# Optimization experiments

Hardware: AMD Instinct MI355X
Metric: run time of the kernel (lower is better)

Reference implementation:

```python
import jax, jax.numpy as jnp
import numpy as np

N = 10000        # nodes
E = 160000       # edges (before self loops)
F_IN = 4         # n_features
D = 128          # d_model (per-head out channels for GAT, GCN width)
H = 8            # n_heads
NEG_SLOPE = 0.2  # PyG GATConv default leaky relu slope


def setup_inputs() -> dict:
    key = jax.random.key(0)
    ks = jax.random.split(key, 10)
    x = jax.random.normal(ks[0], (N, F_IN), dtype=jnp.float32)
    edge_index = jax.random.randint(ks[1], (2, E), 0, N, dtype=jnp.int64)
    s = 0.05
    gat_w = jax.random.normal(ks[2], (F_IN, H * D), dtype=jnp.float32) * s
    att_src = jax.random.normal(ks[3], (H, D), dtype=jnp.float32) * s
    att_dst = jax.random.normal(ks[4], (H, D), dtype=jnp.float32) * s
    gat_b = jnp.zeros((H * D,), dtype=jnp.float32)
    gcn1_w = jax.random.normal(ks[5], (H * D, D), dtype=jnp.float32) * s
    gcn1_b = jnp.zeros((D,), dtype=jnp.float32)
    gcn2_w = jax.random.normal(ks[6], (D, D), dtype=jnp.float32) * s
    gcn2_b = jnp.zeros((D,), dtype=jnp.float32)
    return {"x": x, "edge_index": edge_index, "gat_w": gat_w,
            "att_src": att_src, "att_dst": att_dst, "gat_b": gat_b,
            "gcn1_w": gcn1_w, "gcn1_b": gcn1_b,
            "gcn2_w": gcn2_w, "gcn2_b": gcn2_b}


def _add_self_loops(edge_index, n):
    loops = jnp.arange(n, dtype=edge_index.dtype)
    src = jnp.concatenate([edge_index[0], loops])
    dst = jnp.concatenate([edge_index[1], loops])
    return src, dst


def _gat_conv(x, src, dst, w, att_src, att_dst, b):
    # PyG GATConv, concat=True: h [N,H,D]
    h = (x @ w).reshape(-1, H, D)
    a_s = jnp.einsum('nhd,hd->nh', h, att_src)   # per-node src score
    a_d = jnp.einsum('nhd,hd->nh', h, att_dst)   # per-node dst score
    e = jax.nn.leaky_relu(a_s[src] + a_d[dst], NEG_SLOPE)  # [Etot,H]
    # segment softmax over destination node, per head
    m = jax.ops.segment_max(e, dst, num_segments=N)
    ex = jnp.exp(e - m[dst])
    denom = jax.ops.segment_sum(ex, dst, num_segments=N)
    alpha = ex / denom[dst]                       # [Etot,H]
    msg = h[src] * alpha[:, :, None]              # [Etot,H,D]
    out = jax.ops.segment_sum(msg, dst, num_segments=N)  # [N,H,D]
    return out.reshape(-1, H * D) + b


def _gcn_conv(x, src, dst, w, b):
    # PyG GCNConv with symmetric normalization (self loops already added)
    h = x @ w
    deg = jax.ops.segment_sum(jnp.ones_like(dst, dtype=h.dtype), dst,
                              num_segments=N)
    dinv = jnp.where(deg > 0, jax.lax.rsqrt(deg), 0.0)
    norm = dinv[src] * dinv[dst]                  # [Etot]
    out = jax.ops.segment_sum(h[src] * norm[:, None], dst, num_segments=N)
    return out + b


def reference(x, edge_index, gat_w, att_src, att_dst, gat_b,
              gcn1_w, gcn1_b, gcn2_w, gcn2_b):
    src, dst = _add_self_loops(edge_index, N)
    h = _gat_conv(x, src, dst, gat_w, att_src, att_dst, gat_b)
    h = jax.nn.gelu(h, approximate=False)         # torch F.gelu is exact erf
    h = _gcn_conv(h, src, dst, gcn1_w, gcn1_b)
    h = jax.nn.gelu(h, approximate=False)
    h = _gcn_conv(h, src, dst, gcn2_w, gcn2_b)
    return h                                      # [N, D]
```

## Files before the change

kernel.cpp:

```cpp
#include <hip/hip_runtime.h>
#include <math.h>

#define HEADS 8
#define DHEAD 128
#define CMODEL 1024
#define BCAP 64

typedef __attribute__((ext_vector_type(8))) short bf16x8;
typedef __attribute__((ext_vector_type(4))) float f32x4;

__device__ __forceinline__ float gelu_exact(float x) {
    return 0.5f * x * (1.0f + erff(x * 0.70710678118654752440f));
}

__device__ __forceinline__ unsigned short f2bf(float f) {
    unsigned u = __float_as_uint(f);
    return (unsigned short)((u + 0x7FFFu + ((u >> 16) & 1u)) >> 16);
}
__device__ __forceinline__ float bf2f(unsigned short h) {
    return __uint_as_float((unsigned)h << 16);
}

__global__ void __launch_bounds__(256) k_scores(const float* __restrict__ x,
                                                const float* __restrict__ gat_w,
                                                const float* __restrict__ att_src,
                                                const float* __restrict__ att_dst,
                                                const float* __restrict__ W1,
                                                const float* __restrict__ W2,
                                                float* __restrict__ xpack,
                                                float* __restrict__ a_d,
                                                int* __restrict__ cursor,
                                                unsigned short* __restrict__ W1hi,
                                                unsigned short* __restrict__ W1lo,
                                                unsigned short* __restrict__ W2hi,
                                                unsigned short* __restrict__ W2lo,
                                                int n_nodes, int nb_scores) {
    if ((int)blockIdx.x >= nb_scores) {
        int t = (blockIdx.x - nb_scores) * 256 + threadIdx.x;
        const int total1 = (1024 >> 5) * 8 * 64;
        const int total2 = (128 >> 5) * 8 * 64;
        const float* W; unsigned short *Whi, *Wlo;
        if (t < total1) { W = W1; Whi = W1hi; Wlo = W1lo; }
        else if (t < total1 + total2) { t -= total1; W = W2; Whi = W2hi; Wlo = W2lo; }
        else return;
        int lane = t & 63;
        int ct = (t >> 6) & 7;
        int kc = t >> 9;
        int quad = lane >> 4;
        int col = ct * 16 + (lane & 15);
        size_t o = (size_t)t * 8;
        #pragma unroll
        for (int j = 0; j < 8; j++) {
            float w = W[(size_t)(kc * 32 + quad * 8 + j) * 128 + col];
            unsigned short h = f2bf(w);
            Whi[o + j] = h;
            Wlo[o + j] = f2bf(w - bf2f(h));
        }
        return;
    }
    __shared__ float ws_s[32], ws_d[32];
    int t = threadIdx.x;
    if (t < 64) {
        int e = t >> 1;
        int which = t & 1;
        int hh = e >> 2, k = e & 3;
        const float* wrow = gat_w + k * CMODEL + hh * DHEAD;
        const float* av = which ? (att_dst + hh * DHEAD) : (att_src + hh * DHEAD);
        float s = 0.0f;
        for (int c = 0; c < DHEAD; c++) s += wrow[c] * av[c];
        if (which) ws_d[e] = s; else ws_s[e] = s;
    }
    int gid = blockIdx.x * 256 + t;
    if (gid < n_nodes) cursor[gid] = 0;
    __syncthreads();
    int p = gid;
    if (p >= n_nodes * HEADS) return;
    int n = p >> 3, hh = p & 7;
    float4 xv = *(const float4*)(x + (size_t)n * 4);
    float4 ws = *(const float4*)&ws_s[hh * 4];
    float4 wd = *(const float4*)&ws_d[hh * 4];
    a_d[p] = xv.x * wd.x + xv.y * wd.y + xv.z * wd.z + xv.w * wd.w;
    xpack[(size_t)n * 16 + 4 + hh] =
        xv.x * ws.x + xv.y * ws.y + xv.z * ws.z + xv.w * ws.w;
    if (hh == 0) *(float4*)(xpack + (size_t)n * 16) = xv;
}

__global__ void __launch_bounds__(256) k_scatter(const int* __restrict__ ei,
                                                 int* __restrict__ cursor,
                                                 int* __restrict__ bucket,
                                                 int n_nodes, int n_edges) {
    int e = blockIdx.x * 256 + threadIdx.x;
    int etot = n_edges + n_nodes;
    if (e >= etot) return;
    int s, d;
    if (e < n_edges) { s = ei[e]; d = ei[n_edges + e]; }
    else             { s = d = e - n_edges; }
    int pos = atomicAdd(&cursor[d], 1);
    if (pos < BCAP) bucket[(d << 6) + pos] = s;
}

__global__ void __launch_bounds__(256) k_smax_out1(const float* __restrict__ xpack,
                                                   const float* __restrict__ a_d,
                                                   const int* __restrict__ deg,
                                                   const int* __restrict__ bucket,
                                                   const float* __restrict__ gat_w,
                                                   const float* __restrict__ bias,
                                                   unsigned short* __restrict__ o_hi,
                                                   unsigned short* __restrict__ o_lo,
                                                   int n_nodes) {
    __shared__ float xs[16 * 32];
    int mb = blockIdx.x;
    int t = threadIdx.x;
    int q = t >> 1;
    int half = t & 1;
    int ln = q >> 3, hh = q & 7;
    int n = mb * 16 + ln;
    float sum = 0.0f;
    float4 acc = make_float4(0, 0, 0, 0);
    if (n < n_nodes) {
        int dg = deg[n]; if (dg > BCAP) dg = BCAP;
        int base = n << 6;
        float ad = a_d[n * 8 + hh];
        int r = half;
        for (; r + 6 < dg; r += 8) {
            int s0 = bucket[base + r + 0], s1 = bucket[base + r + 2];
            int s2 = bucket[base + r + 4], s3 = bucket[base + r + 6];
            const float* p0 = xpack + (size_t)s0 * 16;
            const float* p1 = xpack + (size_t)s1 * 16;
            const float* p2 = xpack + (size_t)s2 * 16;
            const float* p3 = xpack + (size_t)s3 * 16;
            float e0 = p0[4 + hh] + ad, e1 = p1[4 + hh] + ad;
            float e2 = p2[4 + hh] + ad, e3 = p3[4 + hh] + ad;
            float4 x0 = *(const float4*)p0;
            float4 x1 = *(const float4*)p1;
            float4 x2 = *(const float4*)p2;
            float4 x3 = *(const float4*)p3;
            e0 = (e0 > 0.0f) ? e0 : 0.2f * e0;  float w0 = __expf(e0);
            e1 = (e1 > 0.0f) ? e1 : 0.2f * e1;  float w1 = __expf(e1);
            e2 = (e2 > 0.0f) ? e2 : 0.2f * e2;  float w2 = __expf(e2);
            e3 = (e3 > 0.0f) ? e3 : 0.2f * e3;  float w3 = __expf(e3);
            sum += w0 + w1 + w2 + w3;
            acc.x += w0 * x0.x + w1 * x1.x + w2 * x2.x + w3 * x3.x;
            acc.y += w0 * x0.y + w1 * x1.y + w2 * x2.y + w3 * x3.y;
            acc.z += w0 * x0.z + w1 * x1.z + w2 * x2.z + w3 * x3.z;
            acc.w += w0 * x0.w + w1 * x1.w + w2 * x2.w + w3 * x3.w;
        }
        for (; r < dg; r += 2) {
            int s = bucket[base + r];
            const float* ps = xpack + (size_t)s * 16;
            float e = ps[4 + hh] + ad;
            e = (e > 0.0f) ? e : 0.2f * e;
            float ex = __expf(e);
            float4 xv = *(const float4*)ps;
            sum += ex;
            acc.x += ex * xv.x; acc.y += ex * xv.y;
            acc.z += ex * xv.z; acc.w += ex * xv.w;
        }
    }
    sum   += __shfl_down(sum, 1);
    acc.x += __shfl_down(acc.x, 1);
    acc.y += __shfl_down(acc.y, 1);
    acc.z += __shfl_down(acc.z, 1);
    acc.w += __shfl_down(acc.w, 1);
    if (half == 0) {
        float inv = (sum > 0.0f) ? (1.0f / sum) : 0.0f;
        *(float4*)&xs[q * 4] = make_float4(acc.x * inv, acc.y * inv,
                                           acc.z * inv, acc.w * inv);
    }
    __syncthreads();
    int lm = t & 15;
    int cb = t >> 4;
    bool valid = (mb * 16 + lm) < n_nodes;
    const float4* w4 = (const float4*)gat_w;
    const float4* b4 = (const float4*)bias;
    #pragma unroll 4
    for (int i = 0; i < 16; i++) {
        int c4 = cb + 16 * i;
        int hh2 = c4 >> 5;
        float4 xa = make_float4(0, 0, 0, 0);
        if (valid) xa = *(const float4*)&xs[(lm * 8 + hh2) * 4];
        float4 w0 = w4[0 * 256 + c4], w1 = w4[1 * 256 + c4],
               w2 = w4[2 * 256 + c4], w3 = w4[3 * 256 + c4];
        float4 bb = b4[c4];
        float v0 = 0, v1 = 0, v2 = 0, v3 = 0;
        if (valid) {
            v0 = gelu_exact(xa.x * w0.x + xa.y * w1.x + xa.z * w2.x + xa.w * w3.x + bb.x);
            v1 = gelu_exact(xa.x * w0.y + xa.y * w1.y + xa.z * w2.y + xa.w * w3.y + bb.y);
            v2 = gelu_exact(xa.x * w0.z + xa.y * w1.z + xa.z * w2.z + xa.w * w3.z + bb.z);
            v3 = gelu_exact(xa.x * w0.w + xa.y * w1.w + xa.z * w2.w + xa.w * w3.w + bb.w);
        }
        int kc = c4 >> 3;
        int quad = (c4 >> 1) & 3;
        int j0 = (c4 & 1) * 4;
        size_t o = (((size_t)mb * 32 + kc) * 64 + quad * 16 + lm) * 8 + j0;
        ushort4 hv, lv;
        unsigned short h;
        h = f2bf(v0); hv.x = h; lv.x = f2bf(v0 - bf2f(h));
        h = f2bf(v1); hv.y = h; lv.y = f2bf(v1 - bf2f(h));
        h = f2bf(v2); hv.z = h; lv.z = f2bf(v2 - bf2f(h));
        h = f2bf(v3); hv.w = h; lv.w = f2bf(v3 - bf2f(h));
        *(ushort4*)(o_hi + o) = hv;
        *(ushort4*)(o_lo + o) = lv;
    }
}

__global__ void __launch_bounds__(256) k_mm_mfma(const unsigned short* __restrict__ Afrag_hi,
                                                 const unsigned short* __restrict__ Afrag_lo,
                                                 const unsigned short* __restrict__ Bhi,
                                                 const unsigned short* __restrict__ Blo,
                                                 const int* __restrict__ deg_scale,
                                                 float* __restrict__ outp,
                                                 int n_nodes, int n_mtiles,
                                                 int kcn, int kc_count) {
    int lane = threadIdx.x & 63;
    int w = threadIdx.x >> 6;
    int colhalf = w >> 1;
    int mtile = blockIdx.x * 2 + (w & 1);
    if (mtile >= n_mtiles) return;
    int kc_begin = blockIdx.y * kc_count;
    outp += (size_t)blockIdx.y * n_nodes * 128;

    int lm = lane & 15, quad = lane >> 4;
    f32x4 acc[4];
    #pragma unroll
    for (int ct = 0; ct < 4; ct++) acc[ct] = (f32x4){0.0f, 0.0f, 0.0f, 0.0f};

    const unsigned short* ah_p = Afrag_hi + (((size_t)mtile * kcn + kc_begin) * 64 + lane) * 8;
    const unsigned short* al_p = Afrag_lo + (((size_t)mtile * kcn + kc_begin) * 64 + lane) * 8;
    const unsigned short* bh_p = Bhi + (((size_t)kc_begin * 8 + colhalf * 4) * 64 + lane) * 8;
    const unsigned short* bl_p = Blo + (((size_t)kc_begin * 8 + colhalf * 4) * 64 + lane) * 8;

    #pragma unroll 4
    for (int kci = 0; kci < kc_count; kci++) {
        bf16x8 ah = *(const bf16x8*)(ah_p + (size_t)kci * 512);
        bf16x8 al = *(const bf16x8*)(al_p + (size_t)kci * 512);
        #pragma unroll
        for (int ct = 0; ct < 4; ct++) {
            bf16x8 bh = *(const bf16x8*)(bh_p + (size_t)kci * 4096 + ct * 512);
            bf16x8 bl = *(const bf16x8*)(bl_p + (size_t)kci * 4096 + ct * 512);
            acc[ct] = __builtin_amdgcn_mfma_f32_16x16x32_bf16(ah, bh, acc[ct], 0, 0, 0);
            acc[ct] = __builtin_amdgcn_mfma_f32_16x16x32_bf16(al, bh, acc[ct], 0, 0, 0);
            acc[ct] = __builtin_amdgcn_mfma_f32_16x16x32_bf16(ah, bl, acc[ct], 0, 0, 0);
        }
    }
    #pragma unroll
    for (int ct = 0; ct < 4; ct++) {
        int col = (colhalf * 4 + ct) * 16 + lm;
        #pragma unroll
        for (int reg = 0; reg < 4; reg++) {
            int row = mtile * 16 + quad * 4 + reg;
            if (row < n_nodes) {
                float v = acc[ct][reg];
                if (deg_scale) v *= 1.0f / sqrtf((float)deg_scale[row]);
                outp[(size_t)row * 128 + col] = v;
            }
        }
    }
}

__global__ void __launch_bounds__(256) k_gcn_agg(const float* __restrict__ t,
                                                 const int* __restrict__ deg,
                                                 const int* __restrict__ bucket,
                                                 const float* __restrict__ bias,
                                                 float* __restrict__ outF,
                                                 unsigned short* __restrict__ outHi,
                                                 unsigned short* __restrict__ outLo,
                                                 int n_nodes, int mode) {
    int c = threadIdx.x & 31;
    int ln = threadIdx.x >> 5;
    int n = blockIdx.x * 8 + ln;
    int col0 = blockIdx.y * 64;
    if (n >= n_nodes) return;
    float2 acc = make_float2(0.0f, 0.0f);
    int dgt = deg[n];
    int dg = dgt > BCAP ? BCAP : dgt;
    int base = n << 6;
    const float* tp = t + col0 + c * 2;
    int r = 0;
    for (; r + 4 <= dg; r += 4) {
        int s0 = bucket[base + r + 0], s1 = bucket[base + r + 1];
        int s2 = bucket[base + r + 2], s3 = bucket[base + r + 3];
        float2 v0 = *(const float2*)(tp + (size_t)s0 * 128);
        float2 v1 = *(const float2*)(tp + (size_t)s1 * 128);
        float2 v2 = *(const float2*)(tp + (size_t)s2 * 128);
        float2 v3 = *(const float2*)(tp + (size_t)s3 * 128);
        acc.x += v0.x + v1.x + v2.x + v3.x;
        acc.y += v0.y + v1.y + v2.y + v3.y;
    }
    for (; r < dg; r++) {
        int s = bucket[base + r];
        float2 v = *(const float2*)(tp + (size_t)s * 128);
        acc.x += v.x; acc.y += v.y;
    }
    float dn = 1.0f / sqrtf((float)dgt);
    int k = col0 + c * 2;
    float2 bb = *(const float2*)(bias + k);
    float vx = acc.x * dn + bb.x;
    float vy = acc.y * dn + bb.y;
    if (mode) {
        vx = gelu_exact(vx); vy = gelu_exact(vy);
        size_t o = (((size_t)(n >> 4) * 4 + (k >> 5)) * 64
                    + ((k >> 3) & 3) * 16 + (n & 15)) * 8 + (k & 7);
        unsigned short hx = f2bf(vx), hy = f2bf(vy);
        outHi[o] = hx; outHi[o + 1] = hy;
        outLo[o] = f2bf(vx - bf2f(hx));
        outLo[o + 1] = f2bf(vy - bf2f(hy));
    } else {
        *(float2*)(outF + (size_t)n * 128 + k) = make_float2(vx, vy);
    }
}

extern "C" void kernel_launch(void* const* d_in, const int* in_sizes, int n_in,
                              void* d_out, int out_size, void* d_ws, size_t ws_size,
                              hipStream_t stream) {
    const float* x        = (const float*)d_in[0];
    const int*   ei       = (const int*)d_in[1];
    const float* gat_w    = (const float*)d_in[2];
    const float* att_src  = (const float*)d_in[3];
    const float* att_dst  = (const float*)d_in[4];
    const float* gat_b    = (const float*)d_in[5];
    const float* gcn1_w   = (const float*)d_in[6];
    const float* gcn1_b   = (const float*)d_in[7];
    const float* gcn2_w   = (const float*)d_in[8];
    const float* gcn2_b   = (const float*)d_in[9];
    float* out = (float*)d_out;

    int N = in_sizes[0] / 4;
    int E = in_sizes[1] / 2;
    int Etot = E + N;
    int n_mtiles = (N + 15) / 16;

    char* base = (char*)d_ws;
    float*          t      = (float*)(base);
    float*          t2     = (float*)(base + 5120000);
    unsigned short* out2hi = (unsigned short*)(base + 10240000);
    unsigned short* out2lo = (unsigned short*)(base + 12800000);
    unsigned short* w1hi   = (unsigned short*)(base + 26000000);
    unsigned short* w1lo   = (unsigned short*)(base + 26262144);
    unsigned short* w2hi   = (unsigned short*)(base + 26524288);
    unsigned short* w2lo   = (unsigned short*)(base + 26557056);
    unsigned short* out1hi = (unsigned short*)(base + 40960000);
    unsigned short* out1lo = (unsigned short*)(base + 61440000);
    size_t off = 81920000;
    float* xpack  = (float*)(base + off); off += (size_t)N * 16 * 4;
    float* a_d    = (float*)(base + off); off += (size_t)N * 8 * 4;
    int*   cursor = (int*)(base + off);   off += (size_t)N * 4;
    int*   bucket = (int*)(base + off);   off += (size_t)N * BCAP * 4;

    int nb_scores = (N * HEADS + 255) / 256;
    int nb_wswz   = (16384 + 2048 + 255) / 256;

    k_scores<<<nb_scores + nb_wswz, 256, 0, stream>>>(x, gat_w, att_src, att_dst,
                                                      gcn1_w, gcn2_w, xpack, a_d, cursor,
                                                      w1hi, w1lo, w2hi, w2lo, N, nb_scores);

    k_scatter<<<(Etot + 255) / 256, 256, 0, stream>>>(ei, cursor, bucket, N, E);

    k_smax_out1<<<n_mtiles, 256, 0, stream>>>(xpack, a_d, cursor, bucket,
                                              gat_w, gat_b, out1hi, out1lo, N);

    int nmb2 = (n_mtiles + 1) / 2;
    int nagg = (N + 7) / 8;

    k_mm_mfma<<<dim3(nmb2, 1), 256, 0, stream>>>(out1hi, out1lo, w1hi, w1lo,
                                                 cursor, t, N, n_mtiles, 32, 32);

    k_gcn_agg<<<dim3(nagg, 2), 256, 0, stream>>>(t, cursor, bucket, gcn1_b,
                                                 nullptr, out2hi, out2lo, N, 1);

    k_mm_mfma<<<dim3(nmb2, 1), 256, 0, stream>>>(out2hi, out2lo, w2hi, w2lo,
                                                 cursor, t2, N, n_mtiles, 4, 4);

    k_gcn_agg<<<dim3(nagg, 2), 256, 0, stream>>>(t2, cursor, bucket, gcn2_b,
                                                 out, nullptr, nullptr, N, 0);
}
```

Measured before the change: 184.5 us.

## Fuse GAT softmax/projection output directly into GCN1 MFMA matmul

The GAT aggregation kernel now computes the 1024-wide GELU activations in 32-column chunks in shared memory and feeds them straight into bf16 split-precision MFMA against the GCN1 weights, writing the degree-scaled result. This removes the round trip of writing and rereading the large hi/lo bf16 activation buffers and one kernel launch. In exchange, each block does the whole 1024-deep K loop with a barrier per chunk and only one 16-row tile per block, so MFMA utilisation and latency hiding may be lower than in the separate matmul kernel.

```diff
diff --git a/kernel.cpp b/kernel.cpp
--- a/kernel.cpp
+++ b/kernel.cpp
@@ -99,108 +99,134 @@
     if (pos < BCAP) bucket[(d << 6) + pos] = s;
 }
 
-__global__ void __launch_bounds__(256) k_smax_out1(const float* __restrict__ xpack,
-                                                   const float* __restrict__ a_d,
-                                                   const int* __restrict__ deg,
-                                                   const int* __restrict__ bucket,
-                                                   const float* __restrict__ gat_w,
-                                                   const float* __restrict__ bias,
-                                                   unsigned short* __restrict__ o_hi,
-                                                   unsigned short* __restrict__ o_lo,
-                                                   int n_nodes) {
+__global__ void __launch_bounds__(256) k_smax_mm1(const float* __restrict__ xpack,
+                                                  const float* __restrict__ a_d,
+                                                  const int* __restrict__ deg,
+                                                  const int* __restrict__ bucket,
+                                                  const float* __restrict__ gat_w,
+                                                  const float* __restrict__ gat_b,
+                                                  const unsigned short* __restrict__ Bhi,
+                                                  const unsigned short* __restrict__ Blo,
+                                                  float* __restrict__ t,
+                                                  int n_nodes) {
     __shared__ float xs[16 * 32];
+    __shared__ float ck[2][16 * 36];
     int mb = blockIdx.x;
-    int t = threadIdx.x;
-    int q = t >> 1;
-    int half = t & 1;
-    int ln = q >> 3, hh = q & 7;
-    int n = mb * 16 + ln;
-    float sum = 0.0f;
-    float4 acc = make_float4(0, 0, 0, 0);
-    if (n < n_nodes) {
-        int dg = deg[n]; if (dg > BCAP) dg = BCAP;
-        int base = n << 6;
-        float ad = a_d[n * 8 + hh];
-        int r = half;
-        for (; r + 6 < dg; r += 8) {
-            int s0 = bucket[base + r + 0], s1 = bucket[base + r + 2];
-            int s2 = bucket[base + r + 4], s3 = bucket[base + r + 6];
-            const float* p0 = xpack + (size_t)s0 * 16;
-            const float* p1 = xpack + (size_t)s1 * 16;
-            const float* p2 = xpack + (size_t)s2 * 16;
-            const float* p3 = xpack + (size_t)s3 * 16;
-            float e0 = p0[4 + hh] + ad, e1 = p1[4 + hh] + ad;
-            float e2 = p2[4 + hh] + ad, e3 = p3[4 + hh] + ad;
-            float4 x0 = *(const float4*)p0;
-            float4 x1 = *(const float4*)p1;
-            float4 x2 = *(const float4*)p2;
-            float4 x3 = *(const float4*)p3;
-            e0 = (e0 > 0.0f) ? e0 : 0.2f * e0;  float w0 = __expf(e0);
-            e1 = (e1 > 0.0f) ? e1 : 0.2f * e1;  float w1 = __expf(e1);
-            e2 = (e2 > 0.0f) ? e2 : 0.2f * e2;  float w2 = __expf(e2);
-            e3 = (e3 > 0.0f) ? e3 : 0.2f * e3;  float w3 = __expf(e3);
-            sum += w0 + w1 + w2 + w3;
-            acc.x += w0 * x0.x + w1 * x1.x + w2 * x2.x + w3 * x3.x;
-            acc.y += w0 * x0.y + w1 * x1.y + w2 * x2.y + w3 * x3.y;
-            acc.z += w0 * x0.z + w1 * x1.z + w2 * x2.z + w3 * x3.z;
-            acc.w += w0 * x0.w + w1 * x1.w + w2 * x2.w + w3 * x3.w;
-        }
-        for (; r < dg; r += 2) {
-            int s = bucket[base + r];
-            const float* ps = xpack + (size_t)s * 16;
-            float e = ps[4 + hh] + ad;
-            e = (e > 0.0f) ? e : 0.2f * e;
-            float ex = __expf(e);
-            float4 xv = *(const float4*)ps;
-            sum += ex;
-            acc.x += ex * xv.x; acc.y += ex * xv.y;
-            acc.z += ex * xv.z; acc.w += ex * xv.w;
-        }
-    }
-    sum   += __shfl_down(sum, 1);
-    acc.x += __shfl_down(acc.x, 1);
-    acc.y += __shfl_down(acc.y, 1);
-    acc.z += __shfl_down(acc.z, 1);
-    acc.w += __shfl_down(acc.w, 1);
-    if (half == 0) {
-        float inv = (sum > 0.0f) ? (1.0f / sum) : 0.0f;
-        *(float4*)&xs[q * 4] = make_float4(acc.x * inv, acc.y * inv,
-                                           acc.z * inv, acc.w * inv);
+    int tid = threadIdx.x;
+    {
+        int q = tid >> 1;
+        int half = tid & 1;
+        int ln = q >> 3, hh = q & 7;
+        int n = mb * 16 + ln;
+        float sum = 0.0f;
+        float4 acc = make_float4(0, 0, 0, 0);
+        if (n < n_nodes) {
+            int dg = deg[n]; if (dg > BCAP) dg = BCAP;
+            int base = n << 6;
+            float ad = a_d[n * 8 + hh];
+            int r = half;
+            for (; r + 6 < dg; r += 8) {
+                int s0 = bucket[base + r + 0], s1 = bucket[base + r + 2];
+                int s2 = bucket[base + r + 4], s3 = bucket[base + r + 6];
+                const float* p0 = xpack + (size_t)s0 * 16;
+                const float* p1 = xpack + (size_t)s1 * 16;
+                const float* p2 = xpack + (size_t)s2 * 16;
+                const float* p3 = xpack + (size_t)s3 * 16;
+                float e0 = p0[4 + hh] + ad, e1 = p1[4 + hh] + ad;
+                float e2 = p2[4 + hh] + ad, e3 = p3[4 + hh] + ad;
+                float4 x0 = *(const float4*)p0;
+                float4 x1 = *(const float4*)p1;
+                float4 x2 = *(const float4*)p2;
+                float4 x3 = *(const float4*)p3;
+                e0 = (e0 > 0.0f) ? e0 : 0.2f * e0;  float w0 = __expf(e0);
+                e1 = (e1 > 0.0f) ? e1 : 0.2f * e1;  float w1 = __expf(e1);
+                e2 = (e2 > 0.0f) ? e2 : 0.2f * e2;  float w2 = __expf(e2);
+                e3 = (e3 > 0.0f) ? e3 : 0.2f * e3;  float w3 = __expf(e3);
+                sum += w0 + w1 + w2 + w3;
+                acc.x += w0 * x0.x + w1 * x1.x + w2 * x2.x + w3 * x3.x;
+                acc.y += w0 * x0.y + w1 * x1.y + w2 * x2.y + w3 * x3.y;
+                acc.z += w0 * x0.z + w1 * x1.z + w2 * x2.z + w3 * x3.z;
+                acc.w += w0 * x0.w + w1 * x1.w + w2 * x2.w + w3 * x3.w;
+            }
+            for (; r < dg; r += 2) {
+                int s = bucket[base + r];
+                const float* ps = xpack + (size_t)s * 16;
+                float e = ps[4 + hh] + ad;
+                e = (e > 0.0f) ? e : 0.2f * e;
+                float ex = __expf(e);
+                float4 xv = *(const float4*)ps;
+                sum += ex;
+                acc.x += ex * xv.x; acc.y += ex * xv.y;
+                acc.z += ex * xv.z; acc.w += ex * xv.w;
+            }
+        }
+        sum   += __shfl_down(sum, 1);
+        acc.x += __shfl_down(acc.x, 1);
+        acc.y += __shfl_down(acc.y, 1);
+        acc.z += __shfl_down(acc.z, 1);
+        acc.w += __shfl_down(acc.w, 1);
+        if (half == 0) {
+            float inv = (sum > 0.0f) ? (1.0f / sum) : 0.0f;
+            *(float4*)&xs[q * 4] = make_float4(acc.x * inv, acc.y * inv,
+                                               acc.z * inv, acc.w * inv);
+        }
     }
     __syncthreads();
-    int lm = t & 15;
-    int cb = t >> 4;
-    bool valid = (mb * 16 + lm) < n_nodes;
-    const float4* w4 = (const float4*)gat_w;
-    const float4* b4 = (const float4*)bias;
-    #pragma unroll 4
-    for (int i = 0; i < 16; i++) {
-        int c4 = cb + 16 * i;
-        int hh2 = c4 >> 5;
-        float4 xa = make_float4(0, 0, 0, 0);
-        if (valid) xa = *(const float4*)&xs[(lm * 8 + hh2) * 4];
-        float4 w0 = w4[0 * 256 + c4], w1 = w4[1 * 256 + c4],
-               w2 = w4[2 * 256 + c4], w3 = w4[3 * 256 + c4];
-        float4 bb = b4[c4];
-        float v0 = 0, v1 = 0, v2 = 0, v3 = 0;
-        if (valid) {
-            v0 = gelu_exact(xa.x * w0.x + xa.y * w1.x + xa.z * w2.x + xa.w * w3.x + bb.x);
-            v1 = gelu_exact(xa.x * w0.y + xa.y * w1.y + xa.z * w2.y + xa.w * w3.y + bb.y);
-            v2 = gelu_exact(xa.x * w0.z + xa.y * w1.z + xa.z * w2.z + xa.w * w3.z + bb.z);
-            v3 = gelu_exact(xa.x * w0.w + xa.y * w1.w + xa.z * w2.w + xa.w * w3.w + bb.w);
-        }
-        int kc = c4 >> 3;
-        int quad = (c4 >> 1) & 3;
-        int j0 = (c4 & 1) * 4;
-        size_t o = (((size_t)mb * 32 + kc) * 64 + quad * 16 + lm) * 8 + j0;
-        ushort4 hv, lv;
-        unsigned short h;
-        h = f2bf(v0); hv.x = h; lv.x = f2bf(v0 - bf2f(h));
-        h = f2bf(v1); hv.y = h; lv.y = f2bf(v1 - bf2f(h));
-        h = f2bf(v2); hv.z = h; lv.z = f2bf(v2 - bf2f(h));
-        h = f2bf(v3); hv.w = h; lv.w = f2bf(v3 - bf2f(h));
-        *(ushort4*)(o_hi + o) = hv;
-        *(ushort4*)(o_lo + o) = lv;
+    int lane = tid & 63;
+    int w = tid >> 6;
+    int lm = lane & 15, quad = lane >> 4;
+    int cc = tid & 31;
+    int rp = tid >> 5;
+    f32x4 macc[2];
+    macc[0] = (f32x4){0.0f, 0.0f, 0.0f, 0.0f};
+    macc[1] = (f32x4){0.0f, 0.0f, 0.0f, 0.0f};
+    for (int kc = 0; kc < 32; kc++) {
+        int buf = kc & 1;
+        int col = kc * 32 + cc;
+        int hh2 = col >> 7;
+        float w0 = gat_w[col], w1 = gat_w[1024 + col],
+              w2 = gat_w[2048 + col], w3 = gat_w[3072 + col];
+        float bb = gat_b[col];
+        #pragma unroll
+        for (int rr = 0; rr < 2; rr++) {
+            int row = rp * 2 + rr;
+            float4 xa = *(const float4*)&xs[(row * 8 + hh2) * 4];
+            float v = xa.x * w0 + xa.y * w1 + xa.z * w2 + xa.w * w3 + bb;
+            ck[buf][row * 36 + cc] = gelu_exact(v);
+        }
+        __syncthreads();
+        float a[8];
+        *(float4*)&a[0] = *(const float4*)&ck[buf][lm * 36 + quad * 8];
+        *(float4*)&a[4] = *(const float4*)&ck[buf][lm * 36 + quad * 8 + 4];
+        bf16x8 ah, al;
+        #pragma unroll
+        for (int j = 0; j < 8; j++) {
+            unsigned short h = f2bf(a[j]);
+            ah[j] = (short)h;
+            al[j] = (short)f2bf(a[j] - bf2f(h));
+        }
+        #pragma unroll
+        for (int ct = 0; ct < 2; ct++) {
+            const unsigned short* bh_p = Bhi + (((size_t)(kc * 8 + w * 2 + ct)) * 64 + lane) * 8;
+            const unsigned short* bl_p = Blo + (((size_t)(kc * 8 + w * 2 + ct)) * 64 + lane) * 8;
+            bf16x8 bh = *(const bf16x8*)bh_p;
+            bf16x8 bl = *(const bf16x8*)bl_p;
+            macc[ct] = __builtin_amdgcn_mfma_f32_16x16x32_bf16(ah, bh, macc[ct], 0, 0, 0);
+            macc[ct] = __builtin_amdgcn_mfma_f32_16x16x32_bf16(al, bh, macc[ct], 0, 0, 0);
+            macc[ct] = __builtin_amdgcn_mfma_f32_16x16x32_bf16(ah, bl, macc[ct], 0, 0, 0);
+        }
+    }
+    #pragma unroll
+    for (int ct = 0; ct < 2; ct++) {
+        int col = (w * 2 + ct) * 16 + lm;
+        #pragma unroll
+        for (int reg = 0; reg < 4; reg++) {
+            int row = mb * 16 + quad * 4 + reg;
+            if (row < n_nodes) {
+                float dv = 1.0f / sqrtf((float)deg[row]);
+                t[(size_t)row * 128 + col] = macc[ct][reg] * dv;
+            }
+        }
     }
 }
 
@@ -210,28 +236,25 @@
                                                  const unsigned short* __restrict__ Blo,
                                                  const int* __restrict__ deg_scale,
                                                  float* __restrict__ outp,
-                                                 int n_nodes, int n_mtiles,
-                                                 int kcn, int kc_count) {
+                                                 int n_nodes, int n_mtiles, int kcn) {
     int lane = threadIdx.x & 63;
     int w = threadIdx.x >> 6;
     int colhalf = w >> 1;
     int mtile = blockIdx.x * 2 + (w & 1);
     if (mtile >= n_mtiles) return;
-    int kc_begin = blockIdx.y * kc_count;
-    outp += (size_t)blockIdx.y * n_nodes * 128;
 
     int lm = lane & 15, quad = lane >> 4;
     f32x4 acc[4];
     #pragma unroll
     for (int ct = 0; ct < 4; ct++) acc[ct] = (f32x4){0.0f, 0.0f, 0.0f, 0.0f};
 
-    const unsigned short* ah_p = Afrag_hi + (((size_t)mtile * kcn + kc_begin) * 64 + lane) * 8;
-    const unsigned short* al_p = Afrag_lo + (((size_t)mtile * kcn + kc_begin) * 64 + lane) * 8;
-    const unsigned short* bh_p = Bhi + (((size_t)kc_begin * 8 + colhalf * 4) * 64 + lane) * 8;
-    const unsigned short* bl_p = Blo + (((size_t)kc_begin * 8 + colhalf * 4) * 64 + lane) * 8;
+    const unsigned short* ah_p = Afrag_hi + ((size_t)mtile * kcn * 64 + lane) * 8;
+    const unsigned short* al_p = Afrag_lo + ((size_t)mtile * kcn * 64 + lane) * 8;
+    const unsigned short* bh_p = Bhi + ((size_t)(colhalf * 4) * 64 + lane) * 8;
+    const unsigned short* bl_p = Blo + ((size_t)(colhalf * 4) * 64 + lane) * 8;
 
     #pragma unroll 4
-    for (int kci = 0; kci < kc_count; kci++) {
+    for (int kci = 0; kci < kcn; kci++) {
         bf16x8 ah = *(const bf16x8*)(ah_p + (size_t)kci * 512);
         bf16x8 al = *(const bf16x8*)(al_p + (size_t)kci * 512);
         #pragma unroll
@@ -250,8 +273,7 @@
         for (int reg = 0; reg < 4; reg++) {
             int row = mtile * 16 + quad * 4 + reg;
             if (row < n_nodes) {
-                float v = acc[ct][reg];
-                if (deg_scale) v *= 1.0f / sqrtf((float)deg_scale[row]);
+                float v = acc[ct][reg] * (1.0f / sqrtf((float)deg_scale[row]));
                 outp[(size_t)row * 128 + col] = v;
             }
         }
@@ -339,8 +361,6 @@
     unsigned short* w1lo   = (unsigned short*)(base + 26262144);
     unsigned short* w2hi   = (unsigned short*)(base + 26524288);
     unsigned short* w2lo   = (unsigned short*)(base + 26557056);
-    unsigned short* out1hi = (unsigned short*)(base + 40960000);
-    unsigned short* out1lo = (unsigned short*)(base + 61440000);
     size_t off = 81920000;
     float* xpack  = (float*)(base + off); off += (size_t)N * 16 * 4;
     float* a_d    = (float*)(base + off); off += (size_t)N * 8 * 4;
@@ -356,20 +376,17 @@
 
     k_scatter<<<(Etot + 255) / 256, 256, 0, stream>>>(ei, cursor, bucket, N, E);
 
-    k_smax_out1<<<n_mtiles, 256, 0, stream>>>(xpack, a_d, cursor, bucket,
-                                              gat_w, gat_b, out1hi, out1lo, N);
+    k_smax_mm1<<<n_mtiles, 256, 0, stream>>>(xpack, a_d, cursor, bucket,
+                                             gat_w, gat_b, w1hi, w1lo, t, N);
 
     int nmb2 = (n_mtiles + 1) / 2;
     int nagg = (N + 7) / 8;
 
-    k_mm_mfma<<<dim3(nmb2, 1), 256, 0, stream>>>(out1hi, out1lo, w1hi, w1lo,
-                                                 cursor, t, N, n_mtiles, 32, 32);
-
     k_gcn_agg<<<dim3(nagg, 2), 256, 0, stream>>>(t, cursor, bucket, gcn1_b,
                                                  nullptr, out2hi, out2lo, N, 1);
 
     k_mm_mfma<<<dim3(nmb2, 1), 256, 0, stream>>>(out2hi, out2lo, w2hi, w2lo,
-                                                 cursor, t2, N, n_mtiles, 4, 4);
+                                                 cursor, t2, N, n_mtiles, 4);
 
     k_gcn_agg<<<dim3(nagg, 2), 256, 0, stream>>>(t2, cursor, bucket, gcn2_b,
                                                  out, nullptr, nullptr, N, 0);
```

Result: faster. 170.8 us (-7.5%).
